# Kernel optimization log

Measured on AMD Instinct MI355X. Metric: run time of the kernel, lower is better.

The kernel has to match this reference:

```python
import jax, jax.numpy as jnp
import numpy as np

B, T, C, H = 2, 2048, 1024, 16
DH = C // H  # head_size = 64
EPS = 1e-5


def layernorm_axis1(x, gamma, beta):
    # Faithful to the torch code: mean/var over dim 1 (TIME axis), unbiased var.
    mean = jnp.mean(x, axis=1, keepdims=True)
    var = jnp.var(x, axis=1, ddof=1, keepdims=True)
    xhat = (x - mean) / jnp.sqrt(var + EPS)
    return gamma * xhat + beta


def setup_inputs() -> dict:
    key = jax.random.key(0)
    ks = jax.random.split(key, 16)
    s_in = 1.0 / np.sqrt(C)
    s_cat = 1.0 / np.sqrt(H * DH)
    s_ff = 1.0 / np.sqrt(4 * C)
    return {
        "x": jax.random.normal(ks[0], (B, T, C), dtype=jnp.float32),
        # per-head Q/K/V projections (no bias), stacked: [H, C, DH]
        "Wq": jax.random.uniform(ks[1], (H, C, DH), jnp.float32, -s_in, s_in),
        "Wk": jax.random.uniform(ks[2], (H, C, DH), jnp.float32, -s_in, s_in),
        "Wv": jax.random.uniform(ks[3], (H, C, DH), jnp.float32, -s_in, s_in),
        # attention output projection [H*DH, C] + bias
        "Wo": jax.random.uniform(ks[4], (H * DH, C), jnp.float32, -s_cat, s_cat),
        "bo": jax.random.uniform(ks[5], (C,), jnp.float32, -s_cat, s_cat),
        # FFN
        "W1": jax.random.uniform(ks[6], (C, 4 * C), jnp.float32, -s_in, s_in),
        "b1": jax.random.uniform(ks[7], (4 * C,), jnp.float32, -s_in, s_in),
        "W2": jax.random.uniform(ks[8], (4 * C, C), jnp.float32, -s_ff, s_ff),
        "b2": jax.random.uniform(ks[9], (C,), jnp.float32, -s_ff, s_ff),
        # LayerNorm affine params (plain tensors in the original)
        "gamma1": jnp.ones((C,), jnp.float32),
        "beta1": jnp.zeros((C,), jnp.float32),
        "gamma2": jnp.ones((C,), jnp.float32),
        "beta2": jnp.zeros((C,), jnp.float32),
    }


def reference(x, Wq, Wk, Wv, Wo, bo, W1, b1, W2, b2, gamma1, beta1, gamma2, beta2):
    # --- pre-LN attention sublayer ---
    x1 = layernorm_axis1(x, gamma1, beta1)                     # [B,T,C]
    q = jnp.einsum("btc,hcd->bhtd", x1, Wq)                    # [B,H,T,DH]
    k = jnp.einsum("btc,hcd->bhtd", x1, Wk)
    v = jnp.einsum("btc,hcd->bhtd", x1, Wv)
    # NOTE: scaled by full embedding dim C (not head_size) — faithful to source.
    scores = jnp.einsum("bhtd,bhsd->bhts", q, k) * (C ** -0.5)  # [B,H,T,T]
    causal = jnp.tril(jnp.ones((T, T), dtype=bool))
    scores = jnp.where(causal, scores, -jnp.inf)
    wei = jax.nn.softmax(scores, axis=-1)
    attn = jnp.einsum("bhts,bhsd->bhtd", wei, v)               # [B,H,T,DH]
    attn = attn.transpose(0, 2, 1, 3).reshape(B, T, H * DH)    # concat heads
    x = x + attn @ Wo + bo
    # --- pre-LN FFN sublayer ---
    x2 = layernorm_axis1(x, gamma2, beta2)
    h = jax.nn.relu(x2 @ W1 + b1)
    x = x + h @ W2 + b2
    return x
```

## Files before the change

kernel.cpp:

```cpp
#include <hip/hip_runtime.h>
#include <math.h>


#define TDIM 2048
#define BDIM 2
#define CDIM 1024
#define HDIM 16
#define DHE  64
#define QKVS 3072
#define NT   32
#define LNEPS 1e-5f
#define SC2  0.0450842200278f

typedef float f32x4 __attribute__((ext_vector_type(4)));
typedef __bf16 bf16x8 __attribute__((ext_vector_type(8)));
typedef __bf16 bf16x4 __attribute__((ext_vector_type(4)));

__device__ __forceinline__ void gld_lds16(const __bf16* g, __bf16* l) {
  __builtin_amdgcn_global_load_lds(
      (const __attribute__((address_space(1))) void*)g,
      (__attribute__((address_space(3))) void*)l, 16, 0, 0);
}

__global__ __launch_bounds__(256) void ln_stats(const float* __restrict__ x,
                                                float* __restrict__ sumv,
                                                float* __restrict__ sqv) {
  int c = blockIdx.x * 256 + threadIdx.x;
  int b = blockIdx.y;
  int t0 = blockIdx.z * (TDIM / 16);
  const float* xp = x + ((size_t)b * TDIM + t0) * CDIM + c;
  float s = 0.f, q = 0.f;
  for (int t = 0; t < TDIM / 16; ++t) {
    float v = xp[(size_t)t * CDIM];
    s += v;
    q += v * v;
  }
  atomicAdd(&sumv[b * CDIM + c], s);
  atomicAdd(&sqv[b * CDIM + c], q);
}

__global__ __launch_bounds__(256) void ln_apply(const float* __restrict__ x,
    const float* __restrict__ sumv, const float* __restrict__ sqv,
    const float* __restrict__ gamma, const float* __restrict__ beta,
    __bf16* __restrict__ y) {
  size_t i = (size_t)blockIdx.x * 256 + threadIdx.x;
  int c = (int)(i & (CDIM - 1));
  int b = (int)(i >> 21);
  float mean = sumv[b * CDIM + c] * (1.f / TDIM);
  float var = (sqv[b * CDIM + c] - mean * mean * (float)TDIM) * (1.f / (TDIM - 1));
  float rstd = rsqrtf(var + LNEPS);
  y[i] = (__bf16)(gamma[c] * (x[i] - mean) * rstd + beta[c]);
}

__global__ __launch_bounds__(256) void pack_all(
    const float* __restrict__ Wq, const float* __restrict__ Wk,
    const float* __restrict__ Wv, const float* __restrict__ Wo,
    const float* __restrict__ W1, const float* __restrict__ W2,
    __bf16* __restrict__ Wqkvb, __bf16* __restrict__ Wob,
    __bf16* __restrict__ W1b, __bf16* __restrict__ W2b) {
  __shared__ float tile[32][33];
  int t = blockIdx.x;
  int tx = threadIdx.x & 31, ty = threadIdx.x >> 5;
  if (t < 3072) {
    int mat = t >> 10, rem = t & 1023;
    int h = rem >> 6, rr = rem & 63;
    int c0 = (rr & 31) * 32, d0 = (rr >> 5) * 32;
    const float* W = (mat == 0) ? Wq : (mat == 1) ? Wk : Wv;
#pragma unroll
    for (int i = 0; i < 4; ++i)
      tile[ty + i * 8][tx] = W[((size_t)h * CDIM + c0 + ty + i * 8) * DHE + d0 + tx];
    __syncthreads();
#pragma unroll
    for (int i = 0; i < 4; ++i) {
      int n = mat * 1024 + h * 64 + d0 + ty + i * 8;
      Wqkvb[(size_t)n * CDIM + c0 + tx] = (__bf16)tile[tx][ty + i * 8];
    }
  } else {
    const float* in; __bf16* outp; int Cc, R, l;
    if (t < 4096)      { in = Wo; outp = Wob; R = 1024; Cc = 1024; l = t - 3072; }
    else if (t < 8192) { in = W1; outp = W1b; R = 1024; Cc = 4096; l = t - 4096; }
    else               { in = W2; outp = W2b; R = 4096; Cc = 1024; l = t - 8192; }
    int ncx = Cc >> 5;
    int c0 = (l % ncx) * 32, r0 = (l / ncx) * 32;
#pragma unroll
    for (int i = 0; i < 4; ++i)
      tile[ty + i * 8][tx] = in[(size_t)(r0 + ty + i * 8) * Cc + c0 + tx];
    __syncthreads();
#pragma unroll
    for (int i = 0; i < 4; ++i)
      outp[(size_t)(c0 + ty + i * 8) * R + r0 + tx] = (__bf16)tile[tx][ty + i * 8];
  }
}

__global__ __launch_bounds__(256) void transp_v(const __bf16* __restrict__ qkv,
    __bf16* __restrict__ vtb) {
  __shared__ __bf16 tile[32][33];
  int bh = blockIdx.y >> 1, d0 = (blockIdx.y & 1) * 32;
  int b = bh >> 4, h = bh & 15;
  int t0 = blockIdx.x * 32;
  int tx = threadIdx.x & 31, ty = threadIdx.x >> 5;
#pragma unroll
  for (int i = 0; i < 4; ++i)
    tile[ty + i * 8][tx] = qkv[((size_t)b * TDIM + t0 + ty + i * 8) * QKVS + 2048 + h * DHE + d0 + tx];
  __syncthreads();
#pragma unroll
  for (int i = 0; i < 4; ++i)
    vtb[((size_t)bh * 64 + d0 + ty + i * 8) * TDIM + t0 + tx] = tile[tx][ty + i * 8];
}

template<bool BIAS, bool RES, bool RELU, bool OUTBF>
__global__ __launch_bounds__(256) void gemm_bf16(
    const __bf16* __restrict__ Ag, const __bf16* __restrict__ Bg,
    const float* __restrict__ bias, const float* __restrict__ res,
    void* __restrict__ Cm, int M, int N, int K) {
  __shared__ __bf16 As[128 * 32];
  __shared__ __bf16 Bs[128 * 32];
  int tid = threadIdx.x;
  int lane = tid & 63, wid = tid >> 6;
  int wr = wid >> 1, wc = wid & 1;
  int m0 = blockIdx.y * 128, n0 = blockIdx.x * 128;
  int srow = tid >> 2, scol = (tid & 3) * 8;
  int l15 = lane & 15, k8 = (lane >> 4) * 8;

  f32x4 acc[4][4];
#pragma unroll
  for (int m = 0; m < 4; ++m)
#pragma unroll
    for (int n = 0; n < 4; ++n) acc[m][n] = (f32x4){0.f, 0.f, 0.f, 0.f};

  for (int k0 = 0; k0 < K; k0 += 32) {
    __syncthreads();
    gld_lds16(Ag + (size_t)(m0 + srow) * K + k0 + scol,       As + tid * 8);
    gld_lds16(Ag + (size_t)(m0 + 64 + srow) * K + k0 + scol,  As + 2048 + tid * 8);
    gld_lds16(Bg + (size_t)(n0 + srow) * K + k0 + scol,       Bs + tid * 8);
    gld_lds16(Bg + (size_t)(n0 + 64 + srow) * K + k0 + scol,  Bs + 2048 + tid * 8);
    __syncthreads();

    bf16x8 af[4], bf[4];
#pragma unroll
    for (int m = 0; m < 4; ++m)
      af[m] = *(const bf16x8*)(As + (wr * 64 + m * 16 + l15) * 32 + k8);
#pragma unroll
    for (int n = 0; n < 4; ++n)
      bf[n] = *(const bf16x8*)(Bs + (wc * 64 + n * 16 + l15) * 32 + k8);
#pragma unroll
    for (int m = 0; m < 4; ++m)
#pragma unroll
      for (int n = 0; n < 4; ++n)
        acc[m][n] = __builtin_amdgcn_mfma_f32_16x16x32_bf16(af[m], bf[n], acc[m][n], 0, 0, 0);
  }

  int rbase = (lane >> 4) * 4;
#pragma unroll
  for (int m = 0; m < 4; ++m) {
    int row = m0 + wr * 64 + m * 16 + rbase;
#pragma unroll
    for (int n = 0; n < 4; ++n) {
      int col = n0 + wc * 64 + n * 16 + l15;
#pragma unroll
      for (int j = 0; j < 4; ++j) {
        float v = acc[m][n][j];
        size_t off = (size_t)(row + j) * N + col;
        if (BIAS) v += bias[col];
        if (RES)  v += res[off];
        if (RELU) v = fmaxf(v, 0.f);
        if (OUTBF) ((__bf16*)Cm)[off] = (__bf16)v;
        else       ((float*)Cm)[off] = v;
      }
    }
  }
}

template<bool BIAS, bool RELU, bool OUTBF>
__global__ __launch_bounds__(512, 2) void gemm256(
    const __bf16* __restrict__ Ag, const __bf16* __restrict__ Bg,
    const float* __restrict__ bias, void* __restrict__ Cm, void* __restrict__ Cm2,
    int M, int N, int K, int ld, int gnx) {
  __shared__ __align__(16) char lds[131072];
  int tid = threadIdx.x;
  int lane = tid & 63, wid = tid >> 6;
  int wm = wid >> 2, wn = wid & 3;
  int l15 = lane & 15, hi = lane >> 4;

  size_t koff = (size_t)blockIdx.y * K;
  Ag += koff; Bg += koff;
  void* Cuse = blockIdx.y ? Cm2 : Cm;

  int nwg = gridDim.x;
  int q = nwg >> 3, r = nwg & 7;
  int xcd = blockIdx.x & 7, pos = blockIdx.x >> 3;
  int wgid = (xcd < r ? xcd * (q + 1) : r * (q + 1) + (xcd - r) * q) + pos;
  int m0 = (wgid / gnx) * 256, n0 = (wgid % gnx) * 256;

  int sr = tid >> 3;
  int skcol = ((tid & 7) ^ (sr & 7)) << 3;

  const int ac0 = (hi * 16) ^ ((l15 & 7) << 4);
  const int ac1 = ac0 ^ 64;

  f32x4 acc[8][4];
#pragma unroll
  for (int i = 0; i < 8; ++i)
#pragma unroll
    for (int j = 0; j < 4; ++j) acc[i][j] = (f32x4){0.f, 0.f, 0.f, 0.f};

  auto stage = [&](const __bf16* __restrict__ G, int grow0, int k0, char* dst) {
#pragma unroll
    for (int c = 0; c < 2; ++c)
      gld_lds16(G + (size_t)(grow0 + c * 64 + sr) * ld + k0 + skcol,
                (__bf16*)(dst + c * 8192) + (size_t)tid * 8);
  };

  int KT = K >> 6;
  stage(Ag, m0,       0, lds);
  stage(Bg, n0,       0, lds + 32768);
  stage(Ag, m0 + 128, 0, lds + 16384);
  stage(Bg, n0 + 128, 0, lds + 32768 + 16384);
  asm volatile("s_waitcnt vmcnt(4)" ::: "memory");
  __builtin_amdgcn_s_barrier();
  asm volatile("" ::: "memory");

  bf16x8 a[4][2], b[2][2];

#define LOADA(MH) do { \
    const char* Ac_ = lds + (size_t)cur * 65536; \
    int rb_ = (wm * 128 + (MH) * 64 + l15) * 128; \
    _Pragma("unroll") \
    for (int i_ = 0; i_ < 4; ++i_) { \
      a[i_][0] = *(const bf16x8*)(Ac_ + rb_ + i_ * 2048 + ac0); \
      a[i_][1] = *(const bf16x8*)(Ac_ + rb_ + i_ * 2048 + ac1); \
    } } while (0)
#define LOADB(NH) do { \
    const char* Bc_ = lds + (size_t)cur * 65536 + 32768; \
    int rb_ = (wn * 64 + (NH) * 32 + l15) * 128; \
    _Pragma("unroll") \
    for (int j_ = 0; j_ < 2; ++j_) { \
      b[j_][0] = *(const bf16x8*)(Bc_ + rb_ + j_ * 2048 + ac0); \
      b[j_][1] = *(const bf16x8*)(Bc_ + rb_ + j_ * 2048 + ac1); \
    } } while (0)
#define QUAD(MH, NH) do { \
    __builtin_amdgcn_s_setprio(1); \
    _Pragma("unroll") \
    for (int i_ = 0; i_ < 4; ++i_) \
    _Pragma("unroll") \
    for (int j_ = 0; j_ < 2; ++j_) { \
      acc[(MH)*4+i_][(NH)*2+j_] = __builtin_amdgcn_mfma_f32_16x16x32_bf16( \
          a[i_][0], b[j_][0], acc[(MH)*4+i_][(NH)*2+j_], 0, 0, 0); \
      acc[(MH)*4+i_][(NH)*2+j_] = __builtin_amdgcn_mfma_f32_16x16x32_bf16( \
          a[i_][1], b[j_][1], acc[(MH)*4+i_][(NH)*2+j_], 0, 0, 0); \
    } \
    __builtin_amdgcn_s_setprio(0); } while (0)

  for (int kt = 0; kt < KT; ++kt) {
    int cur = kt & 1;
    char* Lnxt = lds + (size_t)(cur ^ 1) * 65536;
    int k1 = (kt + 1) << 6;
    bool notlast = (kt < KT - 1);

    LOADA(0); LOADB(0);
    if (notlast) stage(Ag, m0, k1, Lnxt);
    __builtin_amdgcn_s_barrier();
    asm volatile("" ::: "memory");
    QUAD(0, 0);
    if (notlast) asm volatile("s_waitcnt vmcnt(4)" ::: "memory");
    else         asm volatile("s_waitcnt vmcnt(2)" ::: "memory");
    __builtin_amdgcn_s_barrier();
    asm volatile("" ::: "memory");

    LOADA(1);
    if (notlast) stage(Bg, n0, k1, Lnxt + 32768);
    __builtin_amdgcn_s_barrier();
    asm volatile("" ::: "memory");
    QUAD(1, 0);
    if (notlast) asm volatile("s_waitcnt vmcnt(4)" ::: "memory");
    else         asm volatile("s_waitcnt vmcnt(0)" ::: "memory");
    __builtin_amdgcn_s_barrier();
    asm volatile("" ::: "memory");

    LOADB(1);
    if (notlast) stage(Ag, m0 + 128, k1, Lnxt + 16384);
    __builtin_amdgcn_s_barrier();
    asm volatile("" ::: "memory");
    QUAD(1, 1);
    __builtin_amdgcn_s_barrier();
    asm volatile("" ::: "memory");

    LOADA(0);
    if (notlast) stage(Bg, n0 + 128, k1, Lnxt + 32768 + 16384);
    __builtin_amdgcn_s_barrier();
    asm volatile("" ::: "memory");
    QUAD(0, 1);
    if (notlast) asm volatile("s_waitcnt vmcnt(4)" ::: "memory");
    __builtin_amdgcn_s_barrier();
    asm volatile("" ::: "memory");
  }
#undef LOADA
#undef LOADB
#undef QUAD

#pragma unroll
  for (int fm = 0; fm < 8; ++fm) {
    int row = m0 + wm * 128 + fm * 16 + hi * 4;
#pragma unroll
    for (int fn = 0; fn < 4; ++fn) {
      int col = n0 + wn * 64 + fn * 16 + l15;
#pragma unroll
      for (int j = 0; j < 4; ++j) {
        float v = acc[fm][fn][j];
        size_t off = (size_t)(row + j) * N + col;
        if (BIAS) v += bias[col];
        if (RELU) v = fmaxf(v, 0.f);
        if (OUTBF) ((__bf16*)Cuse)[off] = (__bf16)v;
        else       ((float*)Cuse)[off] = v;
      }
    }
  }
}

__global__ __launch_bounds__(256) void ffn2_reduce(const float* __restrict__ p0,
    const float* __restrict__ p1, const float* __restrict__ b2,
    const float* __restrict__ xmid, float* __restrict__ out) {
  size_t i = ((size_t)blockIdx.x * 256 + threadIdx.x) * 4;
  int c = (int)(i & (CDIM - 1));
  float4 a = *(const float4*)(p0 + i);
  float4 b = *(const float4*)(p1 + i);
  float4 r = *(const float4*)(xmid + i);
  float4 bb = *(const float4*)(b2 + c);
  float4 v;
  v.x = a.x + b.x + r.x + bb.x;
  v.y = a.y + b.y + r.y + bb.y;
  v.z = a.z + b.z + r.z + bb.z;
  v.w = a.w + b.w + r.w + bb.w;
  *(float4*)(out + i) = v;
}

__global__ __launch_bounds__(512, 4) void attn_mfma(const __bf16* __restrict__ qkv,
    const __bf16* __restrict__ vt, __bf16* __restrict__ o) {
  __shared__ __align__(16) char smem[55296];
  __bf16 (*Ks)[64][72] = (__bf16 (*)[64][72])(smem);
  __bf16 (*Vs)[64][72] = (__bf16 (*)[64][72])(smem + 18432);
  __bf16 (*Ps)[16][72] = (__bf16 (*)[16][72])(smem + 36864);
  float (*Os)[64]      = (float (*)[64])(smem);
  float* ms = (float*)(smem + 16384);
  float* ls = (float*)(smem + 16640);

  int bh = blockIdx.y;
  int b = bh >> 4, h = bh & 15;
  int bxA = blockIdx.x;
  int bxB = NT - 1 - bxA;
  int tid = threadIdx.x;
  int lane = tid & 63, w = tid >> 6;
  int wq = w & 3;
  int g = w >> 2;
  int l15 = lane & 15, hi = lane >> 4;
  int hi4 = hi * 4;
  size_t bT = (size_t)b * TDIM;

  bf16x8 onesb;
#pragma unroll
  for (int i = 0; i < 8; ++i) onesb[i] = (l15 == 0) ? (__bf16)1.0f : (__bf16)0.0f;

  bf16x8 qfA[2], qfB[2];
  {
    const __bf16* qp = qkv + (bT + bxA * 64 + wq * 16 + l15) * QKVS + h * DHE;
    qfA[0] = *(const bf16x8*)(qp + hi * 8);
    qfA[1] = *(const bf16x8*)(qp + 32 + hi * 8);
    qp = qkv + (bT + bxB * 64 + wq * 16 + l15) * QKVS + h * DHE;
    qfB[0] = *(const bf16x8*)(qp + hi * 8);
    qfB[1] = *(const bf16x8*)(qp + 32 + hi * 8);
  }

  float mA = -INFINITY, mB = -INFINITY;
  f32x4 lA = (f32x4){0.f, 0.f, 0.f, 0.f};
  f32x4 lB = (f32x4){0.f, 0.f, 0.f, 0.f};
  f32x4 oA[4], oB[4];
#pragma unroll
  for (int n = 0; n < 4; ++n) {
    oA[n] = (f32x4){0.f, 0.f, 0.f, 0.f};
    oB[n] = (f32x4){0.f, 0.f, 0.f, 0.f};
  }

  int g_tid = tid & 255;
  int r0 = g_tid >> 3, c8 = (g_tid & 7) * 8;

  auto process = [&](const bf16x8* qf, float& m_i, f32x4& l_acc, f32x4* oacc,
                     int bx, int t2) {
    f32x4 sacc[4];
#pragma unroll
    for (int n = 0; n < 4; ++n) sacc[n] = (f32x4){0.f, 0.f, 0.f, 0.f};
    __builtin_amdgcn_s_setprio(1);
#pragma unroll
    for (int n = 0; n < 4; ++n)
#pragma unroll
      for (int kk = 0; kk < 2; ++kk) {
        bf16x8 kf = *(const bf16x8*)&Ks[g][n * 16 + l15][kk * 32 + hi * 8];
        sacc[n] = __builtin_amdgcn_mfma_f32_16x16x32_bf16(kf, qf[kk], sacc[n], 0, 0, 0);
      }
    __builtin_amdgcn_s_setprio(0);

    int myq = wq * 16 + l15;
    if (t2 == bx) {
#pragma unroll
      for (int n = 0; n < 4; ++n)
#pragma unroll
        for (int j = 0; j < 4; ++j)
          if (n * 16 + hi4 + j > myq) sacc[n][j] = -INFINITY;
    }

    float mx = sacc[0][0];
#pragma unroll
    for (int n = 0; n < 4; ++n) {
      float a0 = fmaxf(sacc[n][0], sacc[n][1]);
      float a1 = fmaxf(sacc[n][2], sacc[n][3]);
      mx = fmaxf(mx, fmaxf(a0, a1));
    }
    mx = fmaxf(mx, __shfl_xor(mx, 16));
    mx = fmaxf(mx, __shfl_xor(mx, 32));
    mx *= SC2;

    if (!__all(mx - m_i <= 8.0f)) {
      float nm = fmaxf(m_i, mx);
      float al = exp2f(m_i - nm);
      m_i = nm;
#pragma unroll
      for (int r = 0; r < 4; ++r) {
        float ao = __shfl(al, hi4 + r);
        l_acc[r] *= ao;
#pragma unroll
        for (int n = 0; n < 4; ++n) oacc[n][r] *= ao;
      }
    }

    float negm = -m_i;
#pragma unroll
    for (int n = 0; n < 4; ++n) {
      bf16x4 pv;
#pragma unroll
      for (int j = 0; j < 4; ++j)
        pv[j] = (__bf16)exp2f(fmaf(sacc[n][j], SC2, negm));
      *(bf16x4*)&Ps[w][l15][n * 16 + hi4] = pv;
    }

    bf16x8 pa0 = *(const bf16x8*)&Ps[w][l15][hi * 8];
    bf16x8 pa1 = *(const bf16x8*)&Ps[w][l15][32 + hi * 8];
    __builtin_amdgcn_s_setprio(1);
#pragma unroll
    for (int n = 0; n < 4; ++n) {
      bf16x8 vf0 = *(const bf16x8*)&Vs[g][n * 16 + l15][hi * 8];
      bf16x8 vf1 = *(const bf16x8*)&Vs[g][n * 16 + l15][32 + hi * 8];
      oacc[n] = __builtin_amdgcn_mfma_f32_16x16x32_bf16(pa0, vf0, oacc[n], 0, 0, 0);
      oacc[n] = __builtin_amdgcn_mfma_f32_16x16x32_bf16(pa1, vf1, oacc[n], 0, 0, 0);
    }
    l_acc = __builtin_amdgcn_mfma_f32_16x16x32_bf16(pa0, onesb, l_acc, 0, 0, 0);
    l_acc = __builtin_amdgcn_mfma_f32_16x16x32_bf16(pa1, onesb, l_acc, 0, 0, 0);
    __builtin_amdgcn_s_setprio(0);
  };

  for (int j = 0; j <= bxB / 2; ++j) {
    int t2 = 2 * j + g;
    bool have = (t2 <= bxB);
    __syncthreads();
    if (have) {
#pragma unroll
      for (int rr = 0; rr < 2; ++rr) {
        int row = rr * 32 + r0;
        *(bf16x8*)&Ks[g][row][c8] =
            *(const bf16x8*)(qkv + (bT + t2 * 64 + row) * QKVS + 1024 + h * DHE + c8);
        *(bf16x8*)&Vs[g][row][c8] =
            *(const bf16x8*)(vt + ((size_t)bh * 64 + row) * TDIM + t2 * 64 + c8);
      }
    }
    __syncthreads();
    if (t2 <= bxA) process(qfA, mA, lA, oA, bxA, t2);
    if (have)      process(qfB, mB, lB, oB, bxB, t2);
  }

  auto merge = [&](int bx, float m_i, const f32x4& l_acc, f32x4* oacc) {
    float m_o[4], l_o[4];
#pragma unroll
    for (int r = 0; r < 4; ++r) {
      m_o[r] = __shfl(m_i, hi4 + r);
      l_o[r] = __shfl(l_acc[r], lane & 48);
    }
    __syncthreads();
    if (g == 1) {
#pragma unroll
      for (int r = 0; r < 4; ++r) {
        int lrow = wq * 16 + hi4 + r;
        if (l15 == 0) { ms[lrow] = m_o[r]; ls[lrow] = l_o[r]; }
#pragma unroll
        for (int n = 0; n < 4; ++n)
          Os[lrow][n * 16 + l15] = oacc[n][r];
      }
    }
    __syncthreads();
    if (g == 0) {
#pragma unroll
      for (int r = 0; r < 4; ++r) {
        int lrow = wq * 16 + hi4 + r;
        float m1 = ms[lrow], l1 = ls[lrow];
        float mm = fmaxf(m_o[r], m1);
        float e0 = exp2f(m_o[r] - mm), e1 = exp2f(m1 - mm);
        float inv = 1.f / (l_o[r] * e0 + l1 * e1);
        size_t row = bT + bx * 64 + lrow;
#pragma unroll
        for (int n = 0; n < 4; ++n) {
          float v = (oacc[n][r] * e0 + Os[lrow][n * 16 + l15] * e1) * inv;
          o[row * CDIM + h * DHE + n * 16 + l15] = (__bf16)v;
        }
      }
    }
  };
  merge(bxA, mA, lA, oA);
  merge(bxB, mB, lB, oB);
}

extern "C" void kernel_launch(void* const* d_in, const int* in_sizes, int n_in,
                              void* d_out, int out_size, void* d_ws, size_t ws_size,
                              hipStream_t stream) {
  (void)in_sizes; (void)n_in; (void)out_size; (void)ws_size;
  const float* x   = (const float*)d_in[0];
  const float* Wq  = (const float*)d_in[1];
  const float* Wk  = (const float*)d_in[2];
  const float* Wv  = (const float*)d_in[3];
  const float* Wo  = (const float*)d_in[4];
  const float* bo  = (const float*)d_in[5];
  const float* W1  = (const float*)d_in[6];
  const float* b1  = (const float*)d_in[7];
  const float* W2  = (const float*)d_in[8];
  const float* b2  = (const float*)d_in[9];
  const float* g1  = (const float*)d_in[10];
  const float* be1 = (const float*)d_in[11];
  const float* g2  = (const float*)d_in[12];
  const float* be2 = (const float*)d_in[13];
  float* out = (float*)d_out;

  char* wsb = (char*)d_ws;
  const size_t MB = 1024 * 1024;
  __bf16* Wqkvb = (__bf16*)(wsb + 0);
  __bf16* Wob   = (__bf16*)(wsb + 6  * MB);
  __bf16* W1b   = (__bf16*)(wsb + 8  * MB);
  __bf16* W2b   = (__bf16*)(wsb + 16 * MB);
  __bf16* qkvb  = (__bf16*)(wsb + 24 * MB);
  __bf16* hb    = (__bf16*)(wsb + 24 * MB);
  __bf16* vtb   = (__bf16*)(wsb + 48 * MB);
  __bf16* x1b   = (__bf16*)(wsb + 56 * MB);
  __bf16* attnb = (__bf16*)(wsb + 56 * MB);
  float*  xmid  = (float*) (wsb + 64 * MB);
  __bf16* x2b   = (__bf16*)(wsb + 80 * MB);
  float*  stats = (float*) (wsb + 88 * MB);
  float*  p0    = (float*) (wsb + 0);
  float*  p1    = (float*) (wsb + 48 * MB);
  float* sum1 = stats,        *sq1 = stats + 2048;
  float* sum2 = stats + 4096, *sq2 = stats + 6144;

  hipMemsetAsync(stats, 0, 4 * 2048 * sizeof(float), stream);

  pack_all<<<dim3(12288), 256, 0, stream>>>(Wq, Wk, Wv, Wo, W1, W2,
                                            Wqkvb, Wob, W1b, W2b);

  ln_stats<<<dim3(CDIM / 256, BDIM, 16), 256, 0, stream>>>(x, sum1, sq1);
  ln_apply<<<dim3((BDIM * TDIM * CDIM) / 256), 256, 0, stream>>>(x, sum1, sq1, g1, be1, x1b);

  gemm256<false, false, true><<<dim3(192, 1), 512, 0, stream>>>(
      x1b, Wqkvb, nullptr, qkvb, qkvb, 4096, 3072, 1024, 1024, 12);

  transp_v<<<dim3(TDIM / 32, 64), 256, 0, stream>>>(qkvb, vtb);

  attn_mfma<<<dim3(NT / 2, BDIM * HDIM), 512, 0, stream>>>(qkvb, vtb, attnb);

  gemm_bf16<true, true, false, false><<<dim3(8, 32), 256, 0, stream>>>(
      attnb, Wob, bo, x, xmid, 4096, 1024, 1024);

  ln_stats<<<dim3(CDIM / 256, BDIM, 16), 256, 0, stream>>>(xmid, sum2, sq2);
  ln_apply<<<dim3((BDIM * TDIM * CDIM) / 256), 256, 0, stream>>>(xmid, sum2, sq2, g2, be2, x2b);

  gemm256<true, true, true><<<dim3(256, 1), 512, 0, stream>>>(
      x2b, W1b, b1, hb, hb, 4096, 4096, 1024, 1024, 16);

  gemm256<false, false, false><<<dim3(64, 2), 512, 0, stream>>>(
      hb, W2b, nullptr, p0, p1, 4096, 1024, 2048, 4096, 4);
  ffn2_reduce<<<dim3(4096), 256, 0, stream>>>(p0, p1, b2, xmid, out);
}
```

Baseline: 273.0 us.

## Simplify GEMM main loop to one barrier per K-tile with full prefetch

Replaces the four-phase interleaved GEMM loop, which had a barrier and partial vmcnt wait around each quadrant, with a simpler schedule. All four global-to-LDS stages for the next tile are issued at the top of each iteration. All B fragments are loaded once per tile, and the loop ends with a single vmcnt(0) wait and one barrier. This cuts barrier count and redundant B reloads, at the cost of more registers for the B fragments and coarser overlap between loads and MFMA.

```diff
diff --git a/kernel.cpp b/kernel.cpp
--- a/kernel.cpp
+++ b/kernel.cpp
@@ -213,14 +213,13 @@
 
   int KT = K >> 6;
   stage(Ag, m0,       0, lds);
+  stage(Ag, m0 + 128, 0, lds + 16384);
   stage(Bg, n0,       0, lds + 32768);
-  stage(Ag, m0 + 128, 0, lds + 16384);
   stage(Bg, n0 + 128, 0, lds + 32768 + 16384);
-  asm volatile("s_waitcnt vmcnt(4)" ::: "memory");
+  asm volatile("s_waitcnt vmcnt(0)" ::: "memory");
   __builtin_amdgcn_s_barrier();
-  asm volatile("" ::: "memory");
-
-  bf16x8 a[4][2], b[2][2];
+
+  bf16x8 a[4][2], b[4][2];
 
 #define LOADA(MH) do { \
     const char* Ac_ = lds + (size_t)cur * 65536; \
@@ -230,72 +229,50 @@
       a[i_][0] = *(const bf16x8*)(Ac_ + rb_ + i_ * 2048 + ac0); \
       a[i_][1] = *(const bf16x8*)(Ac_ + rb_ + i_ * 2048 + ac1); \
     } } while (0)
-#define LOADB(NH) do { \
+#define LOADBF do { \
     const char* Bc_ = lds + (size_t)cur * 65536 + 32768; \
-    int rb_ = (wn * 64 + (NH) * 32 + l15) * 128; \
+    int rb_ = (wn * 64 + l15) * 128; \
     _Pragma("unroll") \
-    for (int j_ = 0; j_ < 2; ++j_) { \
+    for (int j_ = 0; j_ < 4; ++j_) { \
       b[j_][0] = *(const bf16x8*)(Bc_ + rb_ + j_ * 2048 + ac0); \
       b[j_][1] = *(const bf16x8*)(Bc_ + rb_ + j_ * 2048 + ac1); \
     } } while (0)
 #define QUAD(MH, NH) do { \
-    __builtin_amdgcn_s_setprio(1); \
     _Pragma("unroll") \
     for (int i_ = 0; i_ < 4; ++i_) \
     _Pragma("unroll") \
     for (int j_ = 0; j_ < 2; ++j_) { \
       acc[(MH)*4+i_][(NH)*2+j_] = __builtin_amdgcn_mfma_f32_16x16x32_bf16( \
-          a[i_][0], b[j_][0], acc[(MH)*4+i_][(NH)*2+j_], 0, 0, 0); \
+          a[i_][0], b[(NH)*2+j_][0], acc[(MH)*4+i_][(NH)*2+j_], 0, 0, 0); \
       acc[(MH)*4+i_][(NH)*2+j_] = __builtin_amdgcn_mfma_f32_16x16x32_bf16( \
-          a[i_][1], b[j_][1], acc[(MH)*4+i_][(NH)*2+j_], 0, 0, 0); \
-    } \
-    __builtin_amdgcn_s_setprio(0); } while (0)
+          a[i_][1], b[(NH)*2+j_][1], acc[(MH)*4+i_][(NH)*2+j_], 0, 0, 0); \
+    } } while (0)
 
   for (int kt = 0; kt < KT; ++kt) {
     int cur = kt & 1;
     char* Lnxt = lds + (size_t)(cur ^ 1) * 65536;
     int k1 = (kt + 1) << 6;
-    bool notlast = (kt < KT - 1);
-
-    LOADA(0); LOADB(0);
-    if (notlast) stage(Ag, m0, k1, Lnxt);
+    if (kt < KT - 1) {
+      stage(Ag, m0,       k1, Lnxt);
+      stage(Ag, m0 + 128, k1, Lnxt + 16384);
+      stage(Bg, n0,       k1, Lnxt + 32768);
+      stage(Bg, n0 + 128, k1, Lnxt + 32768 + 16384);
+    }
+    LOADBF;
+    LOADA(0);
+    __builtin_amdgcn_s_setprio(1);
+    QUAD(0, 0); QUAD(0, 1);
+    __builtin_amdgcn_s_setprio(0);
+    LOADA(1);
+    __builtin_amdgcn_s_setprio(1);
+    QUAD(1, 0); QUAD(1, 1);
+    __builtin_amdgcn_s_setprio(0);
+    asm volatile("" ::: "memory");
+    asm volatile("s_waitcnt vmcnt(0)" ::: "memory");
     __builtin_amdgcn_s_barrier();
-    asm volatile("" ::: "memory");
-    QUAD(0, 0);
-    if (notlast) asm volatile("s_waitcnt vmcnt(4)" ::: "memory");
-    else         asm volatile("s_waitcnt vmcnt(2)" ::: "memory");
-    __builtin_amdgcn_s_barrier();
-    asm volatile("" ::: "memory");
-
-    LOADA(1);
-    if (notlast) stage(Bg, n0, k1, Lnxt + 32768);
-    __builtin_amdgcn_s_barrier();
-    asm volatile("" ::: "memory");
-    QUAD(1, 0);
-    if (notlast) asm volatile("s_waitcnt vmcnt(4)" ::: "memory");
-    else         asm volatile("s_waitcnt vmcnt(0)" ::: "memory");
-    __builtin_amdgcn_s_barrier();
-    asm volatile("" ::: "memory");
-
-    LOADB(1);
-    if (notlast) stage(Ag, m0 + 128, k1, Lnxt + 16384);
-    __builtin_amdgcn_s_barrier();
-    asm volatile("" ::: "memory");
-    QUAD(1, 1);
-    __builtin_amdgcn_s_barrier();
-    asm volatile("" ::: "memory");
-
-    LOADA(0);
-    if (notlast) stage(Bg, n0 + 128, k1, Lnxt + 32768 + 16384);
-    __builtin_amdgcn_s_barrier();
-    asm volatile("" ::: "memory");
-    QUAD(0, 1);
-    if (notlast) asm volatile("s_waitcnt vmcnt(4)" ::: "memory");
-    __builtin_amdgcn_s_barrier();
-    asm volatile("" ::: "memory");
   }
 #undef LOADA
-#undef LOADB
+#undef LOADBF
 #undef QUAD
 
 #pragma unroll
```

Result: faster. 257.3 us (-5.7%).
